# Kernel tuning notes

Hardware: AMD Instinct MI355X
Metric: run time of the kernel (lower is better)

Reference implementation:

```python
import jax, jax.numpy as jnp
import numpy as np

T, EQ, N, H, K_HOPS, K_POOL = 4, 4096, 8192, 32, 2, 3


def setup_inputs() -> dict:
    key = jax.random.key(0)
    ks = jax.random.split(key, 6)
    s = 1.0 / np.sqrt(H)
    return {
        "edge_index": jax.random.randint(ks[0], (T, 2, EQ), 0, N),
        "W_gcn": jax.random.normal(ks[1], (1, H), jnp.float32) * 0.5,
        "b_gcn": jnp.zeros((H,), jnp.float32),
        "W_ih": jax.random.normal(ks[2], (3 * H, H), jnp.float32) * s,
        "W_hh": jax.random.normal(ks[3], (3 * H, H), jnp.float32) * s,
        "b_ih": jax.random.normal(ks[4], (3 * H,), jnp.float32) * s,
        "b_hh": jax.random.normal(ks[5], (3 * H,), jnp.float32) * s,
        "num_nodes": N,
    }


def _reach(seeds, src, dst, num_nodes, k):
    # k-hop reachability masks, PyG k_hop_subgraph flow='source_to_target'
    # (walk edges backwards: add sources of edges whose target is reached).
    eq = seeds.shape[0]
    R = jnp.zeros((eq, num_nodes), bool).at[jnp.arange(eq), seeds].set(True)
    for _ in range(k):
        R = R.at[:, src].max(R[:, dst])
    return R


def reference(edge_index, W_gcn, b_gcn, W_ih, W_hh, b_ih, b_hh, num_nodes):
    uq = edge_index[-1, 0]  # [EQ] query-edge sources (last snapshot)
    vq = edge_index[-1, 1]  # [EQ] query-edge targets

    def per_graph(ei):
        src, dst = ei[0], ei[1]
        Ru = _reach(uq, src, dst, num_nodes, K_HOPS)  # [EQ, N]
        Rv = _reach(vq, src, dst, num_nodes, K_HOPS)
        # union of the two k-hop subgraph edge sets (dedup via OR)
        incl = (Ru[:, src] & Ru[:, dst]) | (Rv[:, src] & Rv[:, dst])  # [EQ, Eg]
        # per-node in-degree within the merged subgraph (degree of edge_index[1])
        deg = jnp.zeros((uq.shape[0], num_nodes), jnp.float32)
        deg = deg.at[:, dst].add(incl.astype(jnp.float32))
        # global_sort_pool(k=3): top-3 nodes by the (single) degree feature,
        # zero-padded if the subgraph has <3 positive-degree nodes
        return jax.lax.top_k(deg, K_POOL)[0]  # [EQ, 3]

    tops = jax.vmap(per_graph)(edge_index)  # [T, EQ, 3]

    # GCNConv(1, H) on the 3 pooled nodes (self-loop-normalized: x @ W + b), ReLU
    h = jax.nn.relu(tops[..., None] * W_gcn[0] + b_gcn)  # [T, EQ, 3, H]

    # GRU over T snapshots, batch = EQ*3 pooled nodes
    x_seq = h.reshape(h.shape[0], -1, H)  # [T, EQ*3, H]
    h0 = jnp.zeros((x_seq.shape[1], H), x_seq.dtype)

    def cell(hprev, x):
        gi = x @ W_ih.T + b_ih
        gh = hprev @ W_hh.T + b_hh
        ir, iz, ig = jnp.split(gi, 3, axis=-1)
        hr, hz, hg = jnp.split(gh, 3, axis=-1)
        r = jax.nn.sigmoid(ir + hr)
        z = jax.nn.sigmoid(iz + hz)
        n = jnp.tanh(ig + r * hg)
        hnew = (1.0 - z) * n + z * hprev
        return hnew, None

    hn, _ = jax.lax.scan(cell, h0, x_seq)
    # stacked hidden_list: one [3, H] state per query edge
    return hn.reshape(-1, K_POOL, H)  # [EQ, 3, H]
```

## Files before the change

kernel.cpp:

```cpp
#include <hip/hip_runtime.h>
#include <hip/hip_bf16.h>
#include <math.h>

#define T_SNAP 4
#define EQn 4096
#define Nn 8192
#define Hn 32
#define NWn (Nn/32)
#define CAP 256

typedef __attribute__((ext_vector_type(4))) float f32x4;
typedef __attribute__((ext_vector_type(8))) short s16x8;

__global__ __launch_bounds__(512) void csr_build(const int* __restrict__ ei,
                                                 unsigned* __restrict__ rp,
                                                 unsigned* __restrict__ csr) {
  __shared__ unsigned cnt[Nn];
  __shared__ unsigned wpart[8];
  const int t = blockIdx.x;
  const int tid = threadIdx.x;
  const int lane = tid & 63;
  const int wv = tid >> 6;
  const int* src = ei + t * 2 * EQn;
  const int* dst = src + EQn;

  for (int i = tid; i < Nn; i += 512) cnt[i] = 0u;
  __syncthreads();
  for (int e = tid; e < EQn; e += 512) atomicAdd(&cnt[dst[e]], 1u);
  __syncthreads();

  unsigned loc[16];
  unsigned s = 0u;
  const int base = tid * 16;
#pragma unroll
  for (int i = 0; i < 16; i++) { loc[i] = s; s += cnt[base + i]; }
  unsigned x = s;
#pragma unroll
  for (int off = 1; off < 64; off <<= 1) {
    unsigned y = __shfl_up(x, off);
    if (lane >= off) x += y;
  }
  if (lane == 63) wpart[wv] = x;
  __syncthreads();
  if (tid == 0) {
    unsigned a = 0u;
    for (int i = 0; i < 8; i++) { unsigned v = wpart[i]; wpart[i] = a; a += v; }
  }
  __syncthreads();
  const unsigned excl = wpart[wv] + (x - s);
#pragma unroll
  for (int i = 0; i < 16; i++) {
    unsigned v = excl + loc[i];
    rp[t * (Nn + 1) + base + i] = v;
    cnt[base + i] = v;
  }
  if (tid == 0) rp[t * (Nn + 1) + Nn] = EQn;
  __syncthreads();

  for (int e = tid; e < EQn; e += 512) {
    int d = dst[e];
    unsigned slot = atomicAdd(&cnt[d], 1u);
    csr[t * EQn + slot] = (unsigned)src[e];
  }
}

__global__ __launch_bounds__(128) void reach_topk(const int* __restrict__ ei,
                                                  const unsigned* __restrict__ rp,
                                                  const unsigned* __restrict__ csr,
                                                  float* __restrict__ tops) {
  __shared__ unsigned bits[2][2][NWn];
  __shared__ unsigned short lists[2][2][CAP];
  __shared__ unsigned cnts[2][2];

  const int w = threadIdx.x >> 6;
  const int lane = threadIdx.x & 63;
  const int h = lane >> 5;
  const int l = lane & 31;
  const int gw = blockIdx.x * 2 + w;
  const int t = gw >> 12;
  const int q = gw & (EQn - 1);

  unsigned* bset = bits[w][h];
  unsigned short* lst = lists[w][h];

  for (int i = l; i < NWn; i += 32) bset[i] = 0u;
  const unsigned seed = (unsigned)ei[(T_SNAP - 1) * 2 * EQn + h * EQn + q];
  __syncthreads();
  if (l == 0) {
    bset[seed >> 5] = 1u << (seed & 31);
    lst[0] = (unsigned short)seed;
    cnts[w][h] = 1u;
  }
  __syncthreads();

  const unsigned* rpt = rp + t * (Nn + 1);
  const unsigned* ct = csr + t * EQn;

  {
    const unsigned b0 = rpt[seed], b1 = rpt[seed + 1];
    for (unsigned idx = b0 + l; idx < b1; idx += 32) {
      const unsigned sN = ct[idx];
      const unsigned m = 1u << (sN & 31);
      const unsigned old = atomicOr(&bset[sN >> 5], m);
      if (!(old & m)) {
        unsigned pos = atomicAdd(&cnts[w][h], 1u);
        if (pos < CAP) lst[pos] = (unsigned short)sN;
      }
    }
  }
  __syncthreads();

  {
    const unsigned fe = min(cnts[w][h], (unsigned)CAP);
    for (unsigned i = 1 + l; i < fe; i += 32) {
      const unsigned n = lst[i];
      const unsigned b0 = rpt[n], b1 = rpt[n + 1];
      for (unsigned idx = b0; idx < b1; idx++) {
        const unsigned sN = ct[idx];
        const unsigned m = 1u << (sN & 31);
        const unsigned old = atomicOr(&bset[sN >> 5], m);
        if (!(old & m)) {
          unsigned pos = atomicAdd(&cnts[w][h], 1u);
          if (pos < CAP) lst[pos] = (unsigned short)sN;
        }
      }
    }
  }
  __syncthreads();

  const unsigned* bu = bits[w][0];
  const unsigned* bv = bits[w][1];
  const unsigned cn = min(cnts[w][h], (unsigned)CAP);
  int a0 = 0, a1 = 0, a2 = 0;
  for (unsigned i = l; i < cn; i += 32) {
    const unsigned n = lst[i];
    if (h == 1 && ((bu[n >> 5] >> (n & 31)) & 1u)) continue;
    const bool nv = (bv[n >> 5] >> (n & 31)) & 1u;
    const unsigned b0 = rpt[n], b1 = rpt[n + 1];
    int d = 0;
    for (unsigned idx = b0; idx < b1; idx++) {
      const unsigned sN = ct[idx];
      if (h == 0) {
        const bool su = (bu[sN >> 5] >> (sN & 31)) & 1u;
        const bool sv = (bv[sN >> 5] >> (sN & 31)) & 1u;
        d += (su || (nv && sv)) ? 1 : 0;
      } else {
        d += (bv[sN >> 5] >> (sN & 31)) & 1u;
      }
    }
    a2 = max(a2, min(a1, d)); a1 = max(a1, min(a0, d)); a0 = max(a0, d);
  }

#pragma unroll
  for (int m = 1; m < 64; m <<= 1) {
    const int b0 = __shfl_xor(a0, m);
    const int b1 = __shfl_xor(a1, m);
    const int b2 = __shfl_xor(a2, m);
    const int r0 = max(a0, b0);
    const int r1 = max(min(a0, b0), max(a1, b1));
    const int r2 = max(max(a2, b2), max(min(a1, b0), min(a0, b1)));
    a0 = r0; a1 = r1; a2 = r2;
  }
  if (lane == 0) {
    float* o = tops + (size_t)(t * EQn + q) * 3;
    o[0] = (float)a0;
    o[1] = (float)a1;
    o[2] = (float)a2;
  }
}

__device__ __forceinline__ short f2bfs(float x) {
  __hip_bfloat16 h = __float2bfloat16(x);
  short s;
  __builtin_memcpy(&s, &h, 2);
  return s;
}
__device__ __forceinline__ float sigm(float x) {
  return __builtin_amdgcn_rcpf(1.f + __expf(-x));
}
__device__ __forceinline__ float tanhfast(float x) {
  return 1.f - 2.f * __builtin_amdgcn_rcpf(1.f + __expf(2.f * x));
}

__global__ __launch_bounds__(256) void gru_kernel(
    const float* __restrict__ tops,
    const float* __restrict__ Wg, const float* __restrict__ bg,
    const float* __restrict__ Wih, const float* __restrict__ Whh,
    const float* __restrict__ bih, const float* __restrict__ bhh,
    float* __restrict__ out) {
  __shared__ short hbuf[4][16 * Hn];
  const int w = threadIdx.x >> 6;
  const int lane = threadIdx.x & 63;
  const int quad = lane >> 4;
  const int c = lane & 15;
  const int waveg = blockIdx.x * 4 + w;
  const int rowbase = waveg * 16;

  const f32x4* Wih4 = reinterpret_cast<const f32x4*>(Wih);
  const f32x4* Whh4 = reinterpret_cast<const f32x4*>(Whh);
  s16x8 Bih[6], Bhh[6];
#pragma unroll
  for (int g = 0; g < 6; g++) {
    const int row = g * 16 + c;
    const int v4 = row * (Hn / 4) + quad * 2;
    f32x4 wa = Wih4[v4], wb = Wih4[v4 + 1];
    f32x4 ha = Whh4[v4], hb = Whh4[v4 + 1];
#pragma unroll
    for (int j = 0; j < 4; j++) {
      Bih[g][j] = f2bfs(wa[j]);
      Bih[g][j + 4] = f2bfs(wb[j]);
      Bhh[g][j] = f2bfs(ha[j]);
      Bhh[g][j + 4] = f2bfs(hb[j]);
    }
  }
  const f32x4* Wg4 = reinterpret_cast<const f32x4*>(Wg);
  const f32x4* bg4 = reinterpret_cast<const f32x4*>(bg);
  f32x4 wga = Wg4[quad * 2], wgb = Wg4[quad * 2 + 1];
  f32x4 bga = bg4[quad * 2], bgb = bg4[quad * 2 + 1];
  float wgv[8], bgv[8];
#pragma unroll
  for (int j = 0; j < 4; j++) {
    wgv[j] = wga[j]; wgv[j + 4] = wgb[j];
    bgv[j] = bga[j]; bgv[j + 4] = bgb[j];
  }
  float bihv[6], bhhv[6];
#pragma unroll
  for (int g = 0; g < 6; g++) {
    bihv[g] = bih[g * 16 + c];
    bhhv[g] = bhh[g * 16 + c];
  }

  f32x4 hc0 = {0.f, 0.f, 0.f, 0.f};
  f32x4 hc1 = {0.f, 0.f, 0.f, 0.f};
  s16x8 hfrag = {0, 0, 0, 0, 0, 0, 0, 0};
  const f32x4 z4 = {0.f, 0.f, 0.f, 0.f};

  for (int t = 0; t < T_SNAP; t++) {
    const float top = tops[t * (EQn * 3) + rowbase + c];
    s16x8 xf;
#pragma unroll
    for (int j = 0; j < 8; j++) {
      float x = top * wgv[j] + bgv[j];
      x = x > 0.f ? x : 0.f;
      xf[j] = f2bfs(x);
    }
    f32x4 gi[6], gh[6];
#pragma unroll
    for (int g = 0; g < 6; g++) {
      gi[g] = __builtin_amdgcn_mfma_f32_16x16x32_bf16(xf, Bih[g], z4, 0, 0, 0);
      gh[g] = __builtin_amdgcn_mfma_f32_16x16x32_bf16(hfrag, Bhh[g], z4, 0, 0, 0);
    }
#pragma unroll
    for (int r = 0; r < 4; r++) {
      float rA = sigm(gi[0][r] + bihv[0] + gh[0][r] + bhhv[0]);
      float zA = sigm(gi[2][r] + bihv[2] + gh[2][r] + bhhv[2]);
      float nA = tanhfast(gi[4][r] + bihv[4] + rA * (gh[4][r] + bhhv[4]));
      hc0[r] = (1.f - zA) * nA + zA * hc0[r];
      float rB = sigm(gi[1][r] + bihv[1] + gh[1][r] + bhhv[1]);
      float zB = sigm(gi[3][r] + bihv[3] + gh[3][r] + bhhv[3]);
      float nB = tanhfast(gi[5][r] + bihv[5] + rB * (gh[5][r] + bhhv[5]));
      hc1[r] = (1.f - zB) * nB + zB * hc1[r];
    }
    if (t < T_SNAP - 1) {
      __syncthreads();
#pragma unroll
      for (int r = 0; r < 4; r++) {
        const int row = quad * 4 + r;
        hbuf[w][row * Hn + c] = f2bfs(hc0[r]);
        hbuf[w][row * Hn + 16 + c] = f2bfs(hc1[r]);
      }
      __syncthreads();
      hfrag = *reinterpret_cast<const s16x8*>(&hbuf[w][c * Hn + quad * 8]);
    }
  }
#pragma unroll
  for (int r = 0; r < 4; r++) {
    const int grow = rowbase + quad * 4 + r;
    out[grow * Hn + c] = hc0[r];
    out[grow * Hn + 16 + c] = hc1[r];
  }
}

extern "C" void kernel_launch(void* const* d_in, const int* in_sizes, int n_in,
                              void* d_out, int out_size, void* d_ws, size_t ws_size,
                              hipStream_t stream) {
  const int* ei = (const int*)d_in[0];
  const float* Wg = (const float*)d_in[1];
  const float* bg = (const float*)d_in[2];
  const float* Wih = (const float*)d_in[3];
  const float* Whh = (const float*)d_in[4];
  const float* bih = (const float*)d_in[5];
  const float* bhh = (const float*)d_in[6];

  unsigned char* ws = (unsigned char*)d_ws;
  unsigned* rp = (unsigned*)ws;
  unsigned* csr = (unsigned*)(ws + (size_t)T_SNAP * (Nn + 1) * 4);
  float* tops = (float*)(ws + (size_t)T_SNAP * (Nn + 1) * 4
                            + (size_t)T_SNAP * EQn * 4);

  csr_build<<<T_SNAP, 512, 0, stream>>>(ei, rp, csr);
  reach_topk<<<(T_SNAP * EQn) / 2, 128, 0, stream>>>(ei, rp, csr, tops);
  gru_kernel<<<(EQn * 3) / 64, 256, 0, stream>>>(tops, Wg, bg, Wih, Whh, bih, bhh,
                                                 (float*)d_out);
}
```

Before: 93.35 us.

## Fuse CSR build, reachability top-k and GRU into one cooperative persistent kernel

Result: slower. 313.2 us (+235.6%).

```diff
diff --git a/kernel.cpp b/kernel.cpp
--- a/kernel.cpp
+++ b/kernel.cpp
@@ -1,6 +1,9 @@
 #include <hip/hip_runtime.h>
+#include <hip/hip_cooperative_groups.h>
 #include <hip/hip_bf16.h>
 #include <math.h>
+
+namespace cg = cooperative_groups;
 
 #define T_SNAP 4
 #define EQn 4096
@@ -11,6 +14,279 @@
 
 typedef __attribute__((ext_vector_type(4))) float f32x4;
 typedef __attribute__((ext_vector_type(8))) short s16x8;
+
+__device__ __forceinline__ short f2bfs(float x) {
+  __hip_bfloat16 h = __float2bfloat16(x);
+  short s;
+  __builtin_memcpy(&s, &h, 2);
+  return s;
+}
+__device__ __forceinline__ float sigm(float x) {
+  return __builtin_amdgcn_rcpf(1.f + __expf(-x));
+}
+__device__ __forceinline__ float tanhfast(float x) {
+  return 1.f - 2.f * __builtin_amdgcn_rcpf(1.f + __expf(2.f * x));
+}
+__device__ __forceinline__ void tfb() { __threadfence_block(); }
+
+__global__ __launch_bounds__(256, 2) void fused_kernel(
+    const int* __restrict__ ei,
+    const float* __restrict__ Wg, const float* __restrict__ bg,
+    const float* __restrict__ Wih, const float* __restrict__ Whh,
+    const float* __restrict__ bih, const float* __restrict__ bhh,
+    unsigned* __restrict__ rp, unsigned* __restrict__ csr,
+    float* __restrict__ tops, float* __restrict__ out) {
+  __shared__ __align__(16) unsigned char smem[32768];
+  __shared__ unsigned wpart[4];
+
+  const int tid = threadIdx.x;
+  const int lane = tid & 63;
+  const int w = tid >> 6;
+  const int nwaves = gridDim.x * 4;
+  const int gw = blockIdx.x * 4 + w;
+
+  if (blockIdx.x < 4) {
+    unsigned* cnt = (unsigned*)smem;
+    const int t = blockIdx.x;
+    const int* src = ei + t * 2 * EQn;
+    const int* dst = src + EQn;
+
+    for (int i = tid; i < Nn; i += 256) cnt[i] = 0u;
+    __syncthreads();
+    for (int e = tid; e < EQn; e += 256) atomicAdd(&cnt[dst[e]], 1u);
+    __syncthreads();
+
+    unsigned loc[32];
+    unsigned s = 0u;
+    const int base = tid * 32;
+#pragma unroll
+    for (int i = 0; i < 32; i++) { loc[i] = s; s += cnt[base + i]; }
+    unsigned x = s;
+#pragma unroll
+    for (int off = 1; off < 64; off <<= 1) {
+      unsigned y = __shfl_up(x, off);
+      if (lane >= off) x += y;
+    }
+    if (lane == 63) wpart[w] = x;
+    __syncthreads();
+    if (tid == 0) {
+      unsigned a = 0u;
+#pragma unroll
+      for (int i = 0; i < 4; i++) { unsigned v = wpart[i]; wpart[i] = a; a += v; }
+    }
+    __syncthreads();
+    const unsigned excl = wpart[w] + (x - s);
+#pragma unroll
+    for (int i = 0; i < 32; i++) {
+      unsigned v = excl + loc[i];
+      rp[t * (Nn + 1) + base + i] = v;
+      cnt[base + i] = v;
+    }
+    if (tid == 0) rp[t * (Nn + 1) + Nn] = EQn;
+    __syncthreads();
+    for (int e = tid; e < EQn; e += 256) {
+      int d = dst[e];
+      unsigned slot = atomicAdd(&cnt[d], 1u);
+      csr[t * EQn + slot] = (unsigned)src[e];
+    }
+  }
+  __threadfence();
+  cg::this_grid().sync();
+
+  {
+    unsigned* bits = (unsigned*)smem;
+    unsigned short* lists = (unsigned short*)(smem + 8192);
+    unsigned* cnts = (unsigned*)(smem + 12288);
+
+    const int h = lane >> 5;
+    const int l = lane & 31;
+
+    unsigned* bu = bits + (w * 2 + 0) * NWn;
+    unsigned* bv = bits + (w * 2 + 1) * NWn;
+    unsigned* bset = bits + (w * 2 + h) * NWn;
+    unsigned short* lst = lists + (w * 2 + h) * CAP;
+    unsigned* cw = cnts + w * 2;
+
+    for (int q = gw; q < EQn; q += nwaves) {
+      const unsigned seed = (unsigned)ei[(T_SNAP - 1) * 2 * EQn + h * EQn + q];
+      for (int t = 0; t < T_SNAP; t++) {
+        const unsigned* rpt = rp + t * (Nn + 1);
+        const unsigned* ct = csr + t * EQn;
+
+        for (int i = l; i < NWn; i += 32) bset[i] = 0u;
+        tfb();
+        if (l == 0) {
+          bset[seed >> 5] = 1u << (seed & 31);
+          lst[0] = (unsigned short)seed;
+          cw[h] = 1u;
+        }
+        tfb();
+        {
+          const unsigned b0 = rpt[seed], b1 = rpt[seed + 1];
+          for (unsigned idx = b0 + l; idx < b1; idx += 32) {
+            const unsigned sN = ct[idx];
+            const unsigned m = 1u << (sN & 31);
+            const unsigned old = atomicOr(&bset[sN >> 5], m);
+            if (!(old & m)) {
+              unsigned pos = atomicAdd(&cw[h], 1u);
+              if (pos < CAP) lst[pos] = (unsigned short)sN;
+            }
+          }
+        }
+        tfb();
+        {
+          const unsigned fe = min(cw[h], (unsigned)CAP);
+          for (unsigned i = 1 + l; i < fe; i += 32) {
+            const unsigned n = lst[i];
+            const unsigned b0 = rpt[n], b1 = rpt[n + 1];
+            for (unsigned idx = b0; idx < b1; idx++) {
+              const unsigned sN = ct[idx];
+              const unsigned m = 1u << (sN & 31);
+              const unsigned old = atomicOr(&bset[sN >> 5], m);
+              if (!(old & m)) {
+                unsigned pos = atomicAdd(&cw[h], 1u);
+                if (pos < CAP) lst[pos] = (unsigned short)sN;
+              }
+            }
+          }
+        }
+        tfb();
+        const unsigned cn = min(cw[h], (unsigned)CAP);
+        int a0 = 0, a1 = 0, a2 = 0;
+        for (unsigned i = l; i < cn; i += 32) {
+          const unsigned n = lst[i];
+          if (h == 1 && ((bu[n >> 5] >> (n & 31)) & 1u)) continue;
+          const bool nv = (bv[n >> 5] >> (n & 31)) & 1u;
+          const unsigned b0 = rpt[n], b1 = rpt[n + 1];
+          int d = 0;
+          for (unsigned idx = b0; idx < b1; idx++) {
+            const unsigned sN = ct[idx];
+            if (h == 0) {
+              const bool su = (bu[sN >> 5] >> (sN & 31)) & 1u;
+              const bool sv = (bv[sN >> 5] >> (sN & 31)) & 1u;
+              d += (su || (nv && sv)) ? 1 : 0;
+            } else {
+              d += (bv[sN >> 5] >> (sN & 31)) & 1u;
+            }
+          }
+          a2 = max(a2, min(a1, d)); a1 = max(a1, min(a0, d)); a0 = max(a0, d);
+        }
+#pragma unroll
+        for (int m = 1; m < 64; m <<= 1) {
+          const int b0 = __shfl_xor(a0, m);
+          const int b1 = __shfl_xor(a1, m);
+          const int b2 = __shfl_xor(a2, m);
+          const int r0 = max(a0, b0);
+          const int r1 = max(min(a0, b0), max(a1, b1));
+          const int r2 = max(max(a2, b2), max(min(a1, b0), min(a0, b1)));
+          a0 = r0; a1 = r1; a2 = r2;
+        }
+        if (lane == 0) {
+          float* o = tops + (size_t)(t * EQn + q) * 3;
+          o[0] = (float)a0;
+          o[1] = (float)a1;
+          o[2] = (float)a2;
+        }
+        tfb();
+      }
+    }
+  }
+  __threadfence();
+  cg::this_grid().sync();
+
+  {
+    short* hbuf = (short*)smem + w * (16 * Hn);
+    const int quad = lane >> 4;
+    const int c = lane & 15;
+
+    const f32x4* Wih4 = reinterpret_cast<const f32x4*>(Wih);
+    const f32x4* Whh4 = reinterpret_cast<const f32x4*>(Whh);
+    s16x8 Bih[6], Bhh[6];
+#pragma unroll
+    for (int g = 0; g < 6; g++) {
+      const int row = g * 16 + c;
+      const int v4 = row * (Hn / 4) + quad * 2;
+      f32x4 wa = Wih4[v4], wb = Wih4[v4 + 1];
+      f32x4 ha = Whh4[v4], hb = Whh4[v4 + 1];
+#pragma unroll
+      for (int j = 0; j < 4; j++) {
+        Bih[g][j] = f2bfs(wa[j]);
+        Bih[g][j + 4] = f2bfs(wb[j]);
+        Bhh[g][j] = f2bfs(ha[j]);
+        Bhh[g][j + 4] = f2bfs(hb[j]);
+      }
+    }
+    const f32x4* Wg4 = reinterpret_cast<const f32x4*>(Wg);
+    const f32x4* bg4 = reinterpret_cast<const f32x4*>(bg);
+    f32x4 wga = Wg4[quad * 2], wgb = Wg4[quad * 2 + 1];
+    f32x4 bga = bg4[quad * 2], bgb = bg4[quad * 2 + 1];
+    float wgv[8], bgv[8];
+#pragma unroll
+    for (int j = 0; j < 4; j++) {
+      wgv[j] = wga[j]; wgv[j + 4] = wgb[j];
+      bgv[j] = bga[j]; bgv[j + 4] = bgb[j];
+    }
+    float bihv[6], bhhv[6];
+#pragma unroll
+    for (int g = 0; g < 6; g++) {
+      bihv[g] = bih[g * 16 + c];
+      bhhv[g] = bhh[g * 16 + c];
+    }
+    const f32x4 z4 = {0.f, 0.f, 0.f, 0.f};
+
+    for (int rg = gw; rg < (EQn * 3) / 16; rg += nwaves) {
+      const int rowbase = rg * 16;
+      f32x4 hc0 = {0.f, 0.f, 0.f, 0.f};
+      f32x4 hc1 = {0.f, 0.f, 0.f, 0.f};
+      s16x8 hfrag = {0, 0, 0, 0, 0, 0, 0, 0};
+
+      for (int t = 0; t < T_SNAP; t++) {
+        const float top = tops[t * (EQn * 3) + rowbase + c];
+        s16x8 xf;
+#pragma unroll
+        for (int j = 0; j < 8; j++) {
+          float x = top * wgv[j] + bgv[j];
+          x = x > 0.f ? x : 0.f;
+          xf[j] = f2bfs(x);
+        }
+        f32x4 gi[6], gh[6];
+#pragma unroll
+        for (int g = 0; g < 6; g++) {
+          gi[g] = __builtin_amdgcn_mfma_f32_16x16x32_bf16(xf, Bih[g], z4, 0, 0, 0);
+          gh[g] = __builtin_amdgcn_mfma_f32_16x16x32_bf16(hfrag, Bhh[g], z4, 0, 0, 0);
+        }
+#pragma unroll
+        for (int r = 0; r < 4; r++) {
+          float rA = sigm(gi[0][r] + bihv[0] + gh[0][r] + bhhv[0]);
+          float zA = sigm(gi[2][r] + bihv[2] + gh[2][r] + bhhv[2]);
+          float nA = tanhfast(gi[4][r] + bihv[4] + rA * (gh[4][r] + bhhv[4]));
+          hc0[r] = (1.f - zA) * nA + zA * hc0[r];
+          float rB = sigm(gi[1][r] + bihv[1] + gh[1][r] + bhhv[1]);
+          float zB = sigm(gi[3][r] + bihv[3] + gh[3][r] + bhhv[3]);
+          float nB = tanhfast(gi[5][r] + bihv[5] + rB * (gh[5][r] + bhhv[5]));
+          hc1[r] = (1.f - zB) * nB + zB * hc1[r];
+        }
+        if (t < T_SNAP - 1) {
+          tfb();
+#pragma unroll
+          for (int r = 0; r < 4; r++) {
+            const int row = quad * 4 + r;
+            hbuf[row * Hn + c] = f2bfs(hc0[r]);
+            hbuf[row * Hn + 16 + c] = f2bfs(hc1[r]);
+          }
+          tfb();
+          hfrag = *reinterpret_cast<const s16x8*>(&hbuf[c * Hn + quad * 8]);
+        }
+      }
+#pragma unroll
+      for (int r = 0; r < 4; r++) {
+        const int grow = rowbase + quad * 4 + r;
+        out[grow * Hn + c] = hc0[r];
+        out[grow * Hn + 16 + c] = hc1[r];
+      }
+    }
+  }
+}
 
 __global__ __launch_bounds__(512) void csr_build(const int* __restrict__ ei,
                                                  unsigned* __restrict__ rp,
@@ -28,7 +304,6 @@
   __syncthreads();
   for (int e = tid; e < EQn; e += 512) atomicAdd(&cnt[dst[e]], 1u);
   __syncthreads();
-
   unsigned loc[16];
   unsigned s = 0u;
   const int base = tid * 16;
@@ -56,7 +331,6 @@
   }
   if (tid == 0) rp[t * (Nn + 1) + Nn] = EQn;
   __syncthreads();
-
   for (int e = tid; e < EQn; e += 512) {
     int d = dst[e];
     unsigned slot = atomicAdd(&cnt[d], 1u);
@@ -95,7 +369,6 @@
 
   const unsigned* rpt = rp + t * (Nn + 1);
   const unsigned* ct = csr + t * EQn;
-
   {
     const unsigned b0 = rpt[seed], b1 = rpt[seed + 1];
     for (unsigned idx = b0 + l; idx < b1; idx += 32) {
@@ -109,7 +382,6 @@
     }
   }
   __syncthreads();
-
   {
     const unsigned fe = min(cnts[w][h], (unsigned)CAP);
     for (unsigned i = 1 + l; i < fe; i += 32) {
@@ -127,7 +399,6 @@
     }
   }
   __syncthreads();
-
   const unsigned* bu = bits[w][0];
   const unsigned* bv = bits[w][1];
   const unsigned cn = min(cnts[w][h], (unsigned)CAP);
@@ -150,7 +421,6 @@
     }
     a2 = max(a2, min(a1, d)); a1 = max(a1, min(a0, d)); a0 = max(a0, d);
   }
-
 #pragma unroll
   for (int m = 1; m < 64; m <<= 1) {
     const int b0 = __shfl_xor(a0, m);
@@ -167,19 +437,6 @@
     o[1] = (float)a1;
     o[2] = (float)a2;
   }
-}
-
-__device__ __forceinline__ short f2bfs(float x) {
-  __hip_bfloat16 h = __float2bfloat16(x);
-  short s;
-  __builtin_memcpy(&s, &h, 2);
-  return s;
-}
-__device__ __forceinline__ float sigm(float x) {
-  return __builtin_amdgcn_rcpf(1.f + __expf(-x));
-}
-__device__ __forceinline__ float tanhfast(float x) {
-  return 1.f - 2.f * __builtin_amdgcn_rcpf(1.f + __expf(2.f * x));
 }
 
 __global__ __launch_bounds__(256) void gru_kernel(
@@ -297,9 +554,24 @@
   unsigned* csr = (unsigned*)(ws + (size_t)T_SNAP * (Nn + 1) * 4);
   float* tops = (float*)(ws + (size_t)T_SNAP * (Nn + 1) * 4
                             + (size_t)T_SNAP * EQn * 4);
-
-  csr_build<<<T_SNAP, 512, 0, stream>>>(ei, rp, csr);
-  reach_topk<<<(T_SNAP * EQn) / 2, 128, 0, stream>>>(ei, rp, csr, tops);
-  gru_kernel<<<(EQn * 3) / 64, 256, 0, stream>>>(tops, Wg, bg, Wih, Whh, bih, bhh,
-                                                 (float*)d_out);
-}
+  float* outp = (float*)d_out;
+
+  void* args[] = {(void*)&ei, (void*)&Wg, (void*)&bg, (void*)&Wih, (void*)&Whh,
+                  (void*)&bih, (void*)&bhh, (void*)&rp, (void*)&csr,
+                  (void*)&tops, (void*)&outp};
+
+  hipError_t err = hipLaunchCooperativeKernel((const void*)fused_kernel,
+                                              dim3(512), dim3(256), args, 0, stream);
+  if (err != hipSuccess) {
+    (void)hipGetLastError();
+    err = hipLaunchCooperativeKernel((const void*)fused_kernel,
+                                     dim3(256), dim3(256), args, 0, stream);
+  }
+  if (err != hipSuccess) {
+    (void)hipGetLastError();
+    csr_build<<<T_SNAP, 512, 0, stream>>>(ei, rp, csr);
+    reach_topk<<<(T_SNAP * EQn) / 2, 128, 0, stream>>>(ei, rp, csr, tops);
+    gru_kernel<<<(EQn * 3) / 64, 256, 0, stream>>>(tops, Wg, bg, Wih, Whh,
+                                                   bih, bhh, outp);
+  }
+}
```
